# Kernel tuning notes

Measured on AMD Instinct MI355X. Metric: run time of the kernel, lower is better.

Reference implementation:

```python
import jax, jax.numpy as jnp
import numpy as np

NUM_CLASSES = 54
EPSILON = 0.001
IMPORTANT = [1, 3, 5, 7, 11, 13, 17, 19, 23, 29, 31, 37]
BATCH = 2_000_000


def setup_inputs() -> dict:
    key = jax.random.key(0)
    k1, k2 = jax.random.split(key)
    logits = jax.random.normal(k1, (BATCH, NUM_CLASSES), dtype=jnp.float32)
    target = jax.random.randint(k2, (BATCH,), 0, NUM_CLASSES, dtype=jnp.int64 if jax.config.read('jax_enable_x64') else jnp.int32)
    important_mask = jnp.zeros((NUM_CLASSES,), dtype=bool).at[jnp.array(IMPORTANT)].set(True)
    return {"logits": logits, "target": target, "important_mask": important_mask}


def reference(logits, target, important_mask):
    # softmax over classes
    sm = jax.nn.softmax(logits, axis=1)                     # [B, C]
    pred = jnp.argmax(sm, axis=1)                           # [B]
    # vectorized membership test (replaces the per-sample .item() loop)
    keep = important_mask[pred] | important_mask[target]    # [B]
    # NLLLoss only reads the target column of log(adjusted_softmax):
    #   kept sample   -> softmax[i, target[i]]
    #   ignored sample-> 1 - (C-1)*epsilon  (constant)
    p_target = jnp.take_along_axis(sm, target[:, None], axis=1)[:, 0]  # [B]
    target_prob = 1.0 - (NUM_CLASSES - 1) * EPSILON
    adj = jnp.where(keep, p_target, target_prob)
    loss = -jnp.mean(jnp.log(adj))
    return loss
```

## Files before the change

kernel.cpp:

```cpp
#include <hip/hip_runtime.h>

#define NCLS 54
#define ROWS 64
#define BATCH_N 2000000

#define IMP_MASK ((1ULL << 1) | (1ULL << 3) | (1ULL << 5) | (1ULL << 7) |   \
                  (1ULL << 11) | (1ULL << 13) | (1ULL << 17) | (1ULL << 19) | \
                  (1ULL << 23) | (1ULL << 29) | (1ULL << 31) | (1ULL << 37))

__global__ __launch_bounds__(64) void loss_main(
    const float* __restrict__ logits,
    const int* __restrict__ target,
    float* __restrict__ partial) {
    __shared__ __align__(16) float tile[ROWS * NCLS];

    const int tid = threadIdx.x;
    const size_t row0 = (size_t)blockIdx.x * ROWS;

    const float4* gp = reinterpret_cast<const float4*>(logits + row0 * NCLS);
    float4* lp = reinterpret_cast<float4*>(tile);
#pragma unroll
    for (int k = 0; k < 13; ++k) {
        lp[tid + 64 * k] = gp[tid + 64 * k];
    }
    if (tid < 864 - 13 * 64) {
        lp[tid + 13 * 64] = gp[tid + 13 * 64];
    }
    int t = target[row0 + tid];
    __syncthreads();

    const float* rv = &tile[tid * NCLS];
    float v[NCLS];
#pragma unroll
    for (int j = 0; j < NCLS / 2; ++j) {
        float2 t2 = reinterpret_cast<const float2*>(rv)[j];
        v[2 * j] = t2.x;
        v[2 * j + 1] = t2.y;
    }
    float vt = rv[t];

    float w[27];
#pragma unroll
    for (int j = 0; j < 27; ++j) w[j] = fmaxf(v[j], v[j + 27]);
#pragma unroll
    for (int j = 0; j < 13; ++j) w[j] = fmaxf(w[j], w[j + 14]);
#pragma unroll
    for (int j = 0; j < 7; ++j) w[j] = fmaxf(w[j], w[j + 7]);
#pragma unroll
    for (int j = 0; j < 3; ++j) w[j] = fmaxf(w[j], w[j + 4]);
    w[0] = fmaxf(w[0], w[2]);
    w[1] = fmaxf(w[1], w[3]);
    const float m = fmaxf(w[0], w[1]);

    const int IMP[12] = {1, 3, 5, 7, 11, 13, 17, 19, 23, 29, 31, 37};
    bool imp_pred = false;
#pragma unroll
    for (int j = 0; j < 12; ++j) imp_pred |= (v[IMP[j]] == m);

    bool keep = imp_pred || (((IMP_MASK >> t) & 1ULL) != 0ULL);

    float s0 = 0.f, s1 = 0.f, s2 = 0.f, s3 = 0.f;
#pragma unroll
    for (int j = 0; j < 52; j += 4) {
        s0 += __expf(v[j]);
        s1 += __expf(v[j + 1]);
        s2 += __expf(v[j + 2]);
        s3 += __expf(v[j + 3]);
    }
    s0 += __expf(v[52]);
    s1 += __expf(v[53]);
    float s = (s0 + s1) + (s2 + s3);

    float local = keep ? (__logf(s) - vt) : 0.054456182f;

#pragma unroll
    for (int off = 32; off > 0; off >>= 1) {
        local += __shfl_down(local, off, 64);
    }
    if (tid == 0) partial[blockIdx.x] = local;
}

__global__ __launch_bounds__(1024) void loss_reduce(
    const float* __restrict__ partial, int n, float* __restrict__ out) {
    float s = 0.f;
    for (int i = threadIdx.x; i < n; i += 1024) s += partial[i];
#pragma unroll
    for (int off = 32; off > 0; off >>= 1) {
        s += __shfl_down(s, off, 64);
    }
    __shared__ float wsum[16];
    int lane = threadIdx.x & 63;
    int wid = threadIdx.x >> 6;
    if (lane == 0) wsum[wid] = s;
    __syncthreads();
    if (threadIdx.x == 0) {
        float bs = 0.f;
#pragma unroll
        for (int k = 0; k < 16; ++k) bs += wsum[k];
        out[0] = bs * (1.0f / (float)BATCH_N);
    }
}

extern "C" void kernel_launch(void* const* d_in, const int* in_sizes, int n_in,
                              void* d_out, int out_size, void* d_ws, size_t ws_size,
                              hipStream_t stream) {
    const float* logits = (const float*)d_in[0];
    const int* target   = (const int*)d_in[1];
    float* out = (float*)d_out;
    float* partial = (float*)d_ws;

    int batch = in_sizes[1];
    int nblocks = batch / ROWS;

    loss_main<<<nblocks, ROWS, 0, stream>>>(logits, target, partial);
    loss_reduce<<<1, 1024, 0, stream>>>(partial, nblocks, out);
}
```

Before: 559.0 us.

## Use persistent blocks with double-buffered async global-to-LDS tile prefetch

Replaces the one-tile-per-block grid with 1280 persistent single-wave blocks. Each block walks over tiles with a stride and keeps one accumulator per thread. The next tile is loaded straight into a second LDS buffer with global_load_lds while the current tile is processed, so load latency overlaps compute and fewer blocks need launching. Correctness relies on the barrier waiting for the async LDS loads to finish. Each CU now has fewer waves in flight, which may limit how much memory latency can be hidden.

```diff
diff --git a/kernel.cpp b/kernel.cpp
--- a/kernel.cpp
+++ b/kernel.cpp
@@ -3,81 +3,102 @@
 #define NCLS 54
 #define ROWS 64
 #define BATCH_N 2000000
+#define NTILES (BATCH_N / ROWS)
+#define TILE_FLOATS (ROWS * NCLS)
+#define NBLOCKS 1280
 
 #define IMP_MASK ((1ULL << 1) | (1ULL << 3) | (1ULL << 5) | (1ULL << 7) |   \
                   (1ULL << 11) | (1ULL << 13) | (1ULL << 17) | (1ULL << 19) | \
                   (1ULL << 23) | (1ULL << 29) | (1ULL << 31) | (1ULL << 37))
 
+typedef __attribute__((address_space(3))) unsigned int lds_u32;
+typedef const __attribute__((address_space(1))) unsigned int glob_u32;
+
 __global__ __launch_bounds__(64) void loss_main(
     const float* __restrict__ logits,
     const int* __restrict__ target,
     float* __restrict__ partial) {
-    __shared__ __align__(16) float tile[ROWS * NCLS];
+    __shared__ __align__(16) float tile[2][TILE_FLOATS];
 
     const int tid = threadIdx.x;
-    const size_t row0 = (size_t)blockIdx.x * ROWS;
 
-    const float4* gp = reinterpret_cast<const float4*>(logits + row0 * NCLS);
-    float4* lp = reinterpret_cast<float4*>(tile);
+    auto prefetch = [&](int t, int buf) {
+        const float* g = logits + (size_t)t * TILE_FLOATS;
 #pragma unroll
-    for (int k = 0; k < 13; ++k) {
-        lp[tid + 64 * k] = gp[tid + 64 * k];
+        for (int c = 0; c < 13; ++c) {
+            __builtin_amdgcn_global_load_lds(
+                (glob_u32*)(g + c * 256 + tid * 4),
+                (lds_u32*)(&tile[buf][c * 256]), 16, 0, 0);
+        }
+        if (tid < 32) {
+            __builtin_amdgcn_global_load_lds(
+                (glob_u32*)(g + 13 * 256 + tid * 4),
+                (lds_u32*)(&tile[buf][13 * 256]), 16, 0, 0);
+        }
+    };
+
+    int t = blockIdx.x;
+    int buf = 0;
+    prefetch(t, 0);
+
+    float acc = 0.0f;
+    for (; t < NTILES; t += NBLOCKS) {
+        __syncthreads();
+
+        const float* rv = &tile[buf][tid * NCLS];
+        float v[NCLS];
+#pragma unroll
+        for (int j = 0; j < NCLS / 2; ++j) {
+            float2 t2 = reinterpret_cast<const float2*>(rv)[j];
+            v[2 * j] = t2.x;
+            v[2 * j + 1] = t2.y;
+        }
+        int tg = target[(size_t)t * ROWS + tid];
+        float vt = rv[tg];
+
+        if (t + NBLOCKS < NTILES) prefetch(t + NBLOCKS, buf ^ 1);
+
+        float w[27];
+#pragma unroll
+        for (int j = 0; j < 27; ++j) w[j] = fmaxf(v[j], v[j + 27]);
+#pragma unroll
+        for (int j = 0; j < 13; ++j) w[j] = fmaxf(w[j], w[j + 14]);
+#pragma unroll
+        for (int j = 0; j < 7; ++j) w[j] = fmaxf(w[j], w[j + 7]);
+#pragma unroll
+        for (int j = 0; j < 3; ++j) w[j] = fmaxf(w[j], w[j + 4]);
+        w[0] = fmaxf(w[0], w[2]);
+        w[1] = fmaxf(w[1], w[3]);
+        const float m = fmaxf(w[0], w[1]);
+
+        const int IMP[12] = {1, 3, 5, 7, 11, 13, 17, 19, 23, 29, 31, 37};
+        bool imp_pred = false;
+#pragma unroll
+        for (int j = 0; j < 12; ++j) imp_pred |= (v[IMP[j]] == m);
+        bool keep = imp_pred || (((IMP_MASK >> tg) & 1ULL) != 0ULL);
+
+        float s0 = 0.f, s1 = 0.f, s2 = 0.f, s3 = 0.f;
+#pragma unroll
+        for (int j = 0; j < 52; j += 4) {
+            s0 += __expf(v[j]);
+            s1 += __expf(v[j + 1]);
+            s2 += __expf(v[j + 2]);
+            s3 += __expf(v[j + 3]);
+        }
+        s0 += __expf(v[52]);
+        s1 += __expf(v[53]);
+        float s = (s0 + s1) + (s2 + s3);
+
+        acc += keep ? (__logf(s) - vt) : 0.054456182f;
+
+        buf ^= 1;
     }
-    if (tid < 864 - 13 * 64) {
-        lp[tid + 13 * 64] = gp[tid + 13 * 64];
-    }
-    int t = target[row0 + tid];
-    __syncthreads();
-
-    const float* rv = &tile[tid * NCLS];
-    float v[NCLS];
-#pragma unroll
-    for (int j = 0; j < NCLS / 2; ++j) {
-        float2 t2 = reinterpret_cast<const float2*>(rv)[j];
-        v[2 * j] = t2.x;
-        v[2 * j + 1] = t2.y;
-    }
-    float vt = rv[t];
-
-    float w[27];
-#pragma unroll
-    for (int j = 0; j < 27; ++j) w[j] = fmaxf(v[j], v[j + 27]);
-#pragma unroll
-    for (int j = 0; j < 13; ++j) w[j] = fmaxf(w[j], w[j + 14]);
-#pragma unroll
-    for (int j = 0; j < 7; ++j) w[j] = fmaxf(w[j], w[j + 7]);
-#pragma unroll
-    for (int j = 0; j < 3; ++j) w[j] = fmaxf(w[j], w[j + 4]);
-    w[0] = fmaxf(w[0], w[2]);
-    w[1] = fmaxf(w[1], w[3]);
-    const float m = fmaxf(w[0], w[1]);
-
-    const int IMP[12] = {1, 3, 5, 7, 11, 13, 17, 19, 23, 29, 31, 37};
-    bool imp_pred = false;
-#pragma unroll
-    for (int j = 0; j < 12; ++j) imp_pred |= (v[IMP[j]] == m);
-
-    bool keep = imp_pred || (((IMP_MASK >> t) & 1ULL) != 0ULL);
-
-    float s0 = 0.f, s1 = 0.f, s2 = 0.f, s3 = 0.f;
-#pragma unroll
-    for (int j = 0; j < 52; j += 4) {
-        s0 += __expf(v[j]);
-        s1 += __expf(v[j + 1]);
-        s2 += __expf(v[j + 2]);
-        s3 += __expf(v[j + 3]);
-    }
-    s0 += __expf(v[52]);
-    s1 += __expf(v[53]);
-    float s = (s0 + s1) + (s2 + s3);
-
-    float local = keep ? (__logf(s) - vt) : 0.054456182f;
 
 #pragma unroll
     for (int off = 32; off > 0; off >>= 1) {
-        local += __shfl_down(local, off, 64);
+        acc += __shfl_down(acc, off, 64);
     }
-    if (tid == 0) partial[blockIdx.x] = local;
+    if (tid == 0) partial[blockIdx.x] = acc;
 }
 
 __global__ __launch_bounds__(1024) void loss_reduce(
@@ -109,9 +130,6 @@
     float* out = (float*)d_out;
     float* partial = (float*)d_ws;
 
-    int batch = in_sizes[1];
-    int nblocks = batch / ROWS;
-
-    loss_main<<<nblocks, ROWS, 0, stream>>>(logits, target, partial);
-    loss_reduce<<<1, 1024, 0, stream>>>(partial, nblocks, out);
+    loss_main<<<NBLOCKS, ROWS, 0, stream>>>(logits, target, partial);
+    loss_reduce<<<1, 1024, 0, stream>>>(partial, NBLOCKS, out);
 }
```

Result: no change. 555.8 us (-0.6%).
